# Optimization experiments

Measured on AMD Instinct MI355X. Metric: run time of the kernel, lower is better.

Reference implementation:

```python
import jax, jax.numpy as jnp
import numpy as np

N_NODES = 100000
N_EDGES = 1600000
D_IN = 128
UNITS = 128


def setup_inputs() -> dict:
    key = jax.random.key(0)
    k1, k2, k3, k4, k5 = jax.random.split(key, 5)
    x = jax.random.normal(k1, (N_NODES, D_IN), dtype=jnp.float32)
    # glorot-uniform-like dense weight
    limit = float(np.sqrt(6.0 / (D_IN + UNITS)))
    w = jax.random.uniform(k2, (D_IN, UNITS), minval=-limit, maxval=limit, dtype=jnp.float32)
    # COO sparse adjacency: A[row, col] = val
    edge_row = jax.random.randint(k3, (N_EDGES,), 0, N_NODES, dtype=jnp.int32)
    edge_col = jax.random.randint(k4, (N_EDGES,), 0, N_NODES, dtype=jnp.int32)
    edge_val = jax.random.uniform(k5, (N_EDGES,), dtype=jnp.float32)
    return {"x": x, "w": w, "edge_row": edge_row, "edge_col": edge_col, "edge_val": edge_val}


def reference(x, w, edge_row, edge_col, edge_val):
    # dropout rate = 0.0 -> identity (module default)
    xw = x @ w                                   # [N, units] dense projection
    # sparse adjacency propagation: out[i] = sum_e val[e] * xw[col[e]] for row[e]==i
    msgs = xw[edge_col] * edge_val[:, None]      # [E, units] irregular gather
    out = jax.ops.segment_sum(msgs, edge_row, num_segments=x.shape[0])
    return jax.nn.relu(out)                      # activation
```

## Files before the change

kernel.cpp:

```cpp
#include <hip/hip_runtime.h>

#define N_NODES 100000
#define N_EDGES 1600000
#define D 128
#define NB 512
#define BCAP 3584
#define BSTRIDE 16
#define CHUNK 4000
#define NSCAT 400
#define NGEMM 782
#define HCAP 1792

typedef __attribute__((ext_vector_type(8))) short  short8;
typedef __attribute__((ext_vector_type(4))) float  floatx4;

__device__ __forceinline__ ushort f2bf(float f) {
    unsigned u = __float_as_uint(f);
    u += 0x7FFF + ((u >> 16) & 1);
    return (ushort)(u >> 16);
}
__device__ __forceinline__ float bf2f(ushort s) {
    return __uint_as_float((unsigned)s << 16);
}
__device__ __forceinline__ int bucket_of(int r)  { return (int)(((unsigned)r << 9) / 100000u); }
__device__ __forceinline__ int row_start(int b)  { return (b * 100000 + 511) >> 9; }

__global__ __launch_bounds__(256) void gemm_xw(const float* __restrict__ x,
                                               const float* __restrict__ w,
                                               ushort* __restrict__ xwb) {
    __shared__ ushort wt[128 * 128];
    __shared__ ushort ct[4][16 * 128];
    const int t    = threadIdx.x;
    const int wv   = t >> 6;
    const int lane = t & 63;
    const int m    = lane & 15;
    const int q    = lane >> 4;

    {
        const float4* w4 = (const float4*)w;
        for (int i = t; i < 4096; i += 256) {
            const float4 v = w4[i];
            const int k = i >> 5;
            const int n = (i & 31) << 2;
            const int c = k >> 3, kc = k & 7;
#pragma unroll
            for (int d = 0; d < 4; ++d) {
                const float val = (d == 0) ? v.x : (d == 1) ? v.y : (d == 2) ? v.z : v.w;
                const int nn = n + d;
                wt[(nn << 7) | (((c ^ (nn & 15)) & 15) << 3) | kc] = f2bf(val);
            }
        }
    }
    __syncthreads();

#pragma unroll
    for (int tile = 0; tile < 2; ++tile) {
        const int rbase = blockIdx.x * 128 + tile * 64 + wv * 16;
        if (rbase >= N_NODES) break;

        const float* xrow = x + (size_t)min(rbase + m, N_NODES - 1) * D;

        floatx4 acc[8];
#pragma unroll
        for (int tt = 0; tt < 8; ++tt) acc[tt] = (floatx4){0.f, 0.f, 0.f, 0.f};

#pragma unroll
        for (int kk = 0; kk < D; kk += 32) {
            const float4 a0 = *(const float4*)(xrow + kk + q * 8);
            const float4 a1 = *(const float4*)(xrow + kk + q * 8 + 4);
            short8 a;
            a[0] = (short)f2bf(a0.x); a[1] = (short)f2bf(a0.y);
            a[2] = (short)f2bf(a0.z); a[3] = (short)f2bf(a0.w);
            a[4] = (short)f2bf(a1.x); a[5] = (short)f2bf(a1.y);
            a[6] = (short)f2bf(a1.z); a[7] = (short)f2bf(a1.w);

#pragma unroll
            for (int tt = 0; tt < 8; ++tt) {
                const int n  = tt * 16 + m;
                const int cc = (((kk >> 3) + q) ^ m) & 15;
                const short8 b = *(const short8*)&wt[(n << 7) | (cc << 3)];
                acc[tt] = __builtin_amdgcn_mfma_f32_16x16x32_bf16(a, b, acc[tt], 0, 0, 0);
            }
        }

#pragma unroll
        for (int tt = 0; tt < 8; ++tt) {
#pragma unroll
            for (int r = 0; r < 4; ++r) {
                ct[wv][((q << 2) | r) * 128 + tt * 16 + m] = f2bf(acc[tt][r]);
            }
        }
        const int rl  = lane >> 2;
        const int ch  = lane & 3;
        const int row = rbase + rl;
        if (row < N_NODES) {
            const ushort* srcp = &ct[wv][rl * 128 + ch * 32];
            ushort*       dstp = &xwb[(size_t)row * D + ch * 32];
#pragma unroll
            for (int u = 0; u < 4; ++u) {
                ((int4*)dstp)[u] = ((const int4*)srcp)[u];
            }
        }
    }
}

__global__ __launch_bounds__(256) void bucket_scatter(const int* __restrict__ erow,
                                                      const int* __restrict__ ecol,
                                                      const float* __restrict__ eval,
                                                      int* __restrict__ bcnt,
                                                      int2* __restrict__ bkt) {
    __shared__ int2  stage[CHUNK];
    __shared__ int   sA[NB], sB[NB], lcur[NB], gbase[NB];
    __shared__ short sbuck[CHUNK];
    const int t  = threadIdx.x;
    const int e0 = blockIdx.x * CHUNK;

    sA[t] = 0; sA[t + 256] = 0;
    __syncthreads();

    for (int i = t; i < CHUNK; i += 256) {
        atomicAdd(&sA[bucket_of(erow[e0 + i])], 1);
    }
    __syncthreads();

    int cur = 0;
    int* bufs[2] = {sA, sB};
#pragma unroll
    for (int o = 1; o < 512; o <<= 1) {
        const int* src = bufs[cur];
        int*       dst = bufs[cur ^ 1];
        const int i0 = t, i1 = t + 256;
        dst[i0] = src[i0] + ((i0 >= o) ? src[i0 - o] : 0);
        dst[i1] = src[i1] + ((i1 >= o) ? src[i1 - o] : 0);
        cur ^= 1;
        __syncthreads();
    }
    {
        const int* incl = bufs[cur];
        int*       excl = bufs[cur ^ 1];
        excl[t]       = (t == 0) ? 0 : incl[t - 1];
        excl[t + 256] = incl[t + 255];
    }
    __syncthreads();
    int* L = bufs[cur ^ 1];

    for (int b = t; b < NB; b += 256) {
        lcur[b] = L[b];
        const int cnt = ((b == NB - 1) ? CHUNK : L[b + 1]) - L[b];
        gbase[b] = (cnt > 0) ? atomicAdd(&bcnt[b * BSTRIDE], cnt) : 0;
    }
    __syncthreads();

    for (int i = t; i < CHUNK; i += 256) {
        const int   r = erow[e0 + i];
        const int   c = ecol[e0 + i];
        const float v = eval[e0 + i];
        const int   b = bucket_of(r);
        const int  rl = r - row_start(b);
        const int pos = atomicAdd(&lcur[b], 1);
        stage[pos] = make_int2((rl << 17) | c, __float_as_int(v));
        sbuck[pos] = (short)b;
    }
    __syncthreads();

    for (int i = t; i < CHUNK; i += 256) {
        const int b   = sbuck[i];
        const int dst = gbase[b] + (i - L[b]);
        if (dst < BCAP) bkt[(size_t)b * BCAP + dst] = stage[i];
    }
}

__global__ __launch_bounds__(256, 4) void csr_gather(const int* __restrict__ bcnt,
                                                     const int2* __restrict__ bkt,
                                                     const ushort* __restrict__ xwb,
                                                     float* __restrict__ out) {
    __shared__ int2 lcsr[HCAP];
    __shared__ int  sA[256], sB[256], lcur[256];
    const int bg = blockIdx.x;
    const int b  = bg >> 1;
    const int h  = bg & 1;
    const int t  = threadIdx.x;
    const int n  = min(bcnt[b * BSTRIDE], BCAP);
    const int r0    = row_start(b);
    const int nrows = row_start(b + 1) - r0;
    const int mid   = (nrows + 1) >> 1;
    const int lo    = h ? mid : 0;
    const int hi    = h ? nrows : mid;
    const int nloc  = hi - lo;

    const int2* src = bkt + (size_t)b * BCAP;
    sA[t] = 0;
    __syncthreads();

    for (int i = t; i < n; i += 256) {
        const int rl = (int)(((unsigned)src[i].x) >> 17);
        if (rl >= lo && rl < hi) atomicAdd(&sA[rl - lo], 1);
    }
    __syncthreads();

    int cur = 0;
    int* bufs[2] = {sA, sB};
#pragma unroll
    for (int o = 1; o < 256; o <<= 1) {
        const int* s = bufs[cur];
        int*       d = bufs[cur ^ 1];
        d[t] = s[t] + ((t >= o) ? s[t - o] : 0);
        cur ^= 1;
        __syncthreads();
    }
    lcur[t] = (t == 0) ? 0 : bufs[cur][t - 1];
    __syncthreads();

    for (int i = t; i < n; i += 256) {
        const int2 e = src[i];
        const int rl = (int)(((unsigned)e.x) >> 17);
        if (rl >= lo && rl < hi) {
            const int pos = atomicAdd(&lcur[rl - lo], 1);
            if (pos < HCAP) lcsr[pos] = make_int2(e.x & 0x1FFFF, e.y);
        }
    }
    __syncthreads();

    const int qid = t >> 4;
    const int lc  = (t & 15) << 3;

    for (int ln = qid; ln < nloc; ln += 16) {
        int start = (ln == 0) ? 0 : lcur[ln - 1];
        int end   = lcur[ln];
        start = min(start, HCAP);
        end   = min(end, HCAP);

        float acc[8] = {0, 0, 0, 0, 0, 0, 0, 0};

        for (int j = start; j < end; j += 4) {
            const int jb = j + 1, jc = j + 2, jd = j + 3;
            const int2 e0 = lcsr[j];
            const int2 e1 = lcsr[min(jb, end - 1)];
            const int2 e2 = lcsr[min(jc, end - 1)];
            const int2 e3 = lcsr[min(jd, end - 1)];
            const short8 m0 = *(const short8*)&xwb[(size_t)e0.x * D + lc];
            const short8 m1 = *(const short8*)&xwb[(size_t)e1.x * D + lc];
            const short8 m2 = *(const short8*)&xwb[(size_t)e2.x * D + lc];
            const short8 m3 = *(const short8*)&xwb[(size_t)e3.x * D + lc];
            const float v0 = __int_as_float(e0.y);
            const float v1 = (jb < end) ? __int_as_float(e1.y) : 0.f;
            const float v2 = (jc < end) ? __int_as_float(e2.y) : 0.f;
            const float v3 = (jd < end) ? __int_as_float(e3.y) : 0.f;
#pragma unroll
            for (int i = 0; i < 8; ++i) {
                acc[i] += v0 * bf2f((ushort)m0[i]);
                acc[i] += v1 * bf2f((ushort)m1[i]);
                acc[i] += v2 * bf2f((ushort)m2[i]);
                acc[i] += v3 * bf2f((ushort)m3[i]);
            }
        }

        float* o = out + (size_t)(r0 + lo + ln) * D + lc;
        *(float4*)(o + 0) = make_float4(fmaxf(acc[0], 0.f), fmaxf(acc[1], 0.f),
                                        fmaxf(acc[2], 0.f), fmaxf(acc[3], 0.f));
        *(float4*)(o + 4) = make_float4(fmaxf(acc[4], 0.f), fmaxf(acc[5], 0.f),
                                        fmaxf(acc[6], 0.f), fmaxf(acc[7], 0.f));
    }
}

extern "C" void kernel_launch(void* const* d_in, const int* in_sizes, int n_in,
                              void* d_out, int out_size, void* d_ws, size_t ws_size,
                              hipStream_t stream) {
    const float* x    = (const float*)d_in[0];
    const float* w    = (const float*)d_in[1];
    const int*   erow = (const int*)d_in[2];
    const int*   ecol = (const int*)d_in[3];
    const float* eval = (const float*)d_in[4];
    float*       out  = (float*)d_out;

    char*   ws_base = (char*)d_ws;
    ushort* xwb  = (ushort*)ws_base;
    int*    bcnt = (int*)(ws_base + 25600000);
    int2*   bkt  = (int2*)(ws_base + 25632768);

    (void)hipMemsetAsync(bcnt, 0, 32768, stream);

    gemm_xw<<<NGEMM, 256, 0, stream>>>(x, w, xwb);
    bucket_scatter<<<NSCAT, 256, 0, stream>>>(erow, ecol, eval, bcnt, bkt);
    csr_gather<<<NB * 2, 256, 0, stream>>>(bcnt, bkt, xwb, out);
}
```

Baseline: 232.0 us.

## Reorder to aggregate-then-project: gather bf16 x, then MFMA GEMM per row tile

After: 225.9 us. 1.03x faster.

```diff
diff --git a/kernel.cpp b/kernel.cpp
--- a/kernel.cpp
+++ b/kernel.cpp
@@ -6,9 +6,9 @@
 #define NB 512
 #define BCAP 3584
 #define BSTRIDE 16
-#define CHUNK 4000
-#define NSCAT 400
-#define NGEMM 782
+#define CHUNK 3200
+#define NSCAT 500
+#define NCAST 521
 #define HCAP 1792
 
 typedef __attribute__((ext_vector_type(8))) short  short8;
@@ -25,94 +25,30 @@
 __device__ __forceinline__ int bucket_of(int r)  { return (int)(((unsigned)r << 9) / 100000u); }
 __device__ __forceinline__ int row_start(int b)  { return (b * 100000 + 511) >> 9; }
 
-__global__ __launch_bounds__(256) void gemm_xw(const float* __restrict__ x,
-                                               const float* __restrict__ w,
-                                               ushort* __restrict__ xwb) {
-    __shared__ ushort wt[128 * 128];
-    __shared__ ushort ct[4][16 * 128];
-    const int t    = threadIdx.x;
-    const int wv   = t >> 6;
-    const int lane = t & 63;
-    const int m    = lane & 15;
-    const int q    = lane >> 4;
-
-    {
-        const float4* w4 = (const float4*)w;
-        for (int i = t; i < 4096; i += 256) {
-            const float4 v = w4[i];
-            const int k = i >> 5;
-            const int n = (i & 31) << 2;
-            const int c = k >> 3, kc = k & 7;
-#pragma unroll
-            for (int d = 0; d < 4; ++d) {
-                const float val = (d == 0) ? v.x : (d == 1) ? v.y : (d == 2) ? v.z : v.w;
-                const int nn = n + d;
-                wt[(nn << 7) | (((c ^ (nn & 15)) & 15) << 3) | kc] = f2bf(val);
-            }
-        }
-    }
-    __syncthreads();
-
-#pragma unroll
-    for (int tile = 0; tile < 2; ++tile) {
-        const int rbase = blockIdx.x * 128 + tile * 64 + wv * 16;
-        if (rbase >= N_NODES) break;
-
-        const float* xrow = x + (size_t)min(rbase + m, N_NODES - 1) * D;
-
-        floatx4 acc[8];
-#pragma unroll
-        for (int tt = 0; tt < 8; ++tt) acc[tt] = (floatx4){0.f, 0.f, 0.f, 0.f};
-
-#pragma unroll
-        for (int kk = 0; kk < D; kk += 32) {
-            const float4 a0 = *(const float4*)(xrow + kk + q * 8);
-            const float4 a1 = *(const float4*)(xrow + kk + q * 8 + 4);
-            short8 a;
-            a[0] = (short)f2bf(a0.x); a[1] = (short)f2bf(a0.y);
-            a[2] = (short)f2bf(a0.z); a[3] = (short)f2bf(a0.w);
-            a[4] = (short)f2bf(a1.x); a[5] = (short)f2bf(a1.y);
-            a[6] = (short)f2bf(a1.z); a[7] = (short)f2bf(a1.w);
-
-#pragma unroll
-            for (int tt = 0; tt < 8; ++tt) {
-                const int n  = tt * 16 + m;
-                const int cc = (((kk >> 3) + q) ^ m) & 15;
-                const short8 b = *(const short8*)&wt[(n << 7) | (cc << 3)];
-                acc[tt] = __builtin_amdgcn_mfma_f32_16x16x32_bf16(a, b, acc[tt], 0, 0, 0);
-            }
-        }
-
-#pragma unroll
-        for (int tt = 0; tt < 8; ++tt) {
-#pragma unroll
-            for (int r = 0; r < 4; ++r) {
-                ct[wv][((q << 2) | r) * 128 + tt * 16 + m] = f2bf(acc[tt][r]);
-            }
-        }
-        const int rl  = lane >> 2;
-        const int ch  = lane & 3;
-        const int row = rbase + rl;
-        if (row < N_NODES) {
-            const ushort* srcp = &ct[wv][rl * 128 + ch * 32];
-            ushort*       dstp = &xwb[(size_t)row * D + ch * 32];
-#pragma unroll
-            for (int u = 0; u < 4; ++u) {
-                ((int4*)dstp)[u] = ((const int4*)srcp)[u];
-            }
-        }
-    }
-}
-
-__global__ __launch_bounds__(256) void bucket_scatter(const int* __restrict__ erow,
-                                                      const int* __restrict__ ecol,
-                                                      const float* __restrict__ eval,
-                                                      int* __restrict__ bcnt,
-                                                      int2* __restrict__ bkt) {
+__global__ __launch_bounds__(256, 4) void cast_and_scatter(const float* __restrict__ x,
+                                                           ushort* __restrict__ xb,
+                                                           const int* __restrict__ erow,
+                                                           const int* __restrict__ ecol,
+                                                           const float* __restrict__ eval,
+                                                           int* __restrict__ bcnt,
+                                                           int2* __restrict__ bkt) {
     __shared__ int2  stage[CHUNK];
     __shared__ int   sA[NB], sB[NB], lcur[NB], gbase[NB];
     __shared__ short sbuck[CHUNK];
-    const int t  = threadIdx.x;
+    const int t = threadIdx.x;
+
+    if (blockIdx.x >= NSCAT) {
+        const int gid = (blockIdx.x - NSCAT) * 256 + t;
+        const float4* x4 = (const float4*)x;
+        for (int i = gid; i < (N_NODES * D / 4); i += NCAST * 256) {
+            const float4 v = x4[i];
+            ushort4 o;
+            o.x = f2bf(v.x); o.y = f2bf(v.y); o.z = f2bf(v.z); o.w = f2bf(v.w);
+            ((ushort4*)xb)[i] = o;
+        }
+        return;
+    }
+
     const int e0 = blockIdx.x * CHUNK;
 
     sA[t] = 0; sA[t + 256] = 0;
@@ -170,12 +106,15 @@
     }
 }
 
-__global__ __launch_bounds__(256, 4) void csr_gather(const int* __restrict__ bcnt,
-                                                     const int2* __restrict__ bkt,
-                                                     const ushort* __restrict__ xwb,
-                                                     float* __restrict__ out) {
-    __shared__ int2 lcsr[HCAP];
-    __shared__ int  sA[256], sB[256], lcur[256];
+__global__ __launch_bounds__(256) void gather_gemm(const int* __restrict__ bcnt,
+                                                   const int2* __restrict__ bkt,
+                                                   const ushort* __restrict__ xb,
+                                                   const float* __restrict__ w,
+                                                   float* __restrict__ out) {
+    __shared__ int2   lcsr[HCAP];
+    __shared__ int    sA[256], sB[256], lcur[256];
+    __shared__ ushort wt[128 * 128];
+    __shared__ ushort gbuf[4][16 * 128];
     const int bg = blockIdx.x;
     const int b  = bg >> 1;
     const int h  = bg & 1;
@@ -188,6 +127,24 @@
     const int hi    = h ? nrows : mid;
     const int nloc  = hi - lo;
 
+    {
+        const float4* w4 = (const float4*)w;
+        const int kb    = t & 7;
+        const int ncol4 = t >> 3;
+        const int nc    = ncol4 << 2;
+        for (int it = 0; it < 16; ++it) {
+            const int k = kb + it * 8;
+            const float4 v = w4[k * 32 + ncol4];
+            const int c = k >> 3, kc = k & 7;
+#pragma unroll
+            for (int d = 0; d < 4; ++d) {
+                const float val = (d == 0) ? v.x : (d == 1) ? v.y : (d == 2) ? v.z : v.w;
+                const int nn = nc + d;
+                wt[(nn << 7) | (((c ^ (nn & 15)) & 15) << 3) | kc] = f2bf(val);
+            }
+        }
+    }
+
     const int2* src = bkt + (size_t)b * BCAP;
     sA[t] = 0;
     __syncthreads();
@@ -221,45 +178,91 @@
     }
     __syncthreads();
 
-    const int qid = t >> 4;
-    const int lc  = (t & 15) << 3;
-
-    for (int ln = qid; ln < nloc; ln += 16) {
-        int start = (ln == 0) ? 0 : lcur[ln - 1];
-        int end   = lcur[ln];
-        start = min(start, HCAP);
-        end   = min(end, HCAP);
-
-        float acc[8] = {0, 0, 0, 0, 0, 0, 0, 0};
-
-        for (int j = start; j < end; j += 4) {
-            const int jb = j + 1, jc = j + 2, jd = j + 3;
-            const int2 e0 = lcsr[j];
-            const int2 e1 = lcsr[min(jb, end - 1)];
-            const int2 e2 = lcsr[min(jc, end - 1)];
-            const int2 e3 = lcsr[min(jd, end - 1)];
-            const short8 m0 = *(const short8*)&xwb[(size_t)e0.x * D + lc];
-            const short8 m1 = *(const short8*)&xwb[(size_t)e1.x * D + lc];
-            const short8 m2 = *(const short8*)&xwb[(size_t)e2.x * D + lc];
-            const short8 m3 = *(const short8*)&xwb[(size_t)e3.x * D + lc];
-            const float v0 = __int_as_float(e0.y);
-            const float v1 = (jb < end) ? __int_as_float(e1.y) : 0.f;
-            const float v2 = (jc < end) ? __int_as_float(e2.y) : 0.f;
-            const float v3 = (jd < end) ? __int_as_float(e3.y) : 0.f;
-#pragma unroll
-            for (int i = 0; i < 8; ++i) {
-                acc[i] += v0 * bf2f((ushort)m0[i]);
-                acc[i] += v1 * bf2f((ushort)m1[i]);
-                acc[i] += v2 * bf2f((ushort)m2[i]);
-                acc[i] += v3 * bf2f((ushort)m3[i]);
-            }
-        }
-
-        float* o = out + (size_t)(r0 + lo + ln) * D + lc;
-        *(float4*)(o + 0) = make_float4(fmaxf(acc[0], 0.f), fmaxf(acc[1], 0.f),
-                                        fmaxf(acc[2], 0.f), fmaxf(acc[3], 0.f));
-        *(float4*)(o + 4) = make_float4(fmaxf(acc[4], 0.f), fmaxf(acc[5], 0.f),
-                                        fmaxf(acc[6], 0.f), fmaxf(acc[7], 0.f));
+    const int wv  = t >> 6;
+    const int ln64 = t & 63;
+    const int qq  = ln64 >> 4;
+    const int m16 = ln64 & 15;
+    const int lc  = m16 << 3;
+    ushort* gb = gbuf[wv];
+    const int base_row = wv * 4;
+    const int IT = (nloc > base_row) ? ((nloc - base_row + 15) >> 4) : 0;
+    const int MBN = (IT + 3) >> 2;
+
+    for (int mb = 0; mb < MBN; ++mb) {
+#pragma unroll
+        for (int j = 0; j < 4; ++j) {
+            const int it = mb * 4 + j;
+            const int ln = base_row + qq + 16 * it;
+
+            float acc[8] = {0, 0, 0, 0, 0, 0, 0, 0};
+            if (ln < nloc) {
+                int start = (ln == 0) ? 0 : lcur[ln - 1];
+                int end   = lcur[ln];
+                start = min(start, HCAP);
+                end   = min(end, HCAP);
+
+                for (int jj = start; jj < end; jj += 4) {
+                    const int jb = jj + 1, jc = jj + 2, jd = jj + 3;
+                    const int2 e0 = lcsr[jj];
+                    const int2 e1 = lcsr[min(jb, end - 1)];
+                    const int2 e2 = lcsr[min(jc, end - 1)];
+                    const int2 e3 = lcsr[min(jd, end - 1)];
+                    const short8 m0 = *(const short8*)&xb[(size_t)e0.x * D + lc];
+                    const short8 m1 = *(const short8*)&xb[(size_t)e1.x * D + lc];
+                    const short8 m2 = *(const short8*)&xb[(size_t)e2.x * D + lc];
+                    const short8 m3 = *(const short8*)&xb[(size_t)e3.x * D + lc];
+                    const float v0 = __int_as_float(e0.y);
+                    const float v1 = (jb < end) ? __int_as_float(e1.y) : 0.f;
+                    const float v2 = (jc < end) ? __int_as_float(e2.y) : 0.f;
+                    const float v3 = (jd < end) ? __int_as_float(e3.y) : 0.f;
+#pragma unroll
+                    for (int i = 0; i < 8; ++i) {
+                        acc[i] += v0 * bf2f((ushort)m0[i]);
+                        acc[i] += v1 * bf2f((ushort)m1[i]);
+                        acc[i] += v2 * bf2f((ushort)m2[i]);
+                        acc[i] += v3 * bf2f((ushort)m3[i]);
+                    }
+                }
+            }
+            const int s    = (j << 2) | qq;
+            const int phys = m16 ^ (s & 7);
+            short8 og;
+#pragma unroll
+            for (int i = 0; i < 8; ++i) og[i] = (short)f2bf(acc[i]);
+            *(short8*)&gb[s * 128 + (phys << 3)] = og;
+        }
+
+        short8 afr[4];
+#pragma unroll
+        for (int k2 = 0; k2 < 4; ++k2) {
+            const int ph = (((k2 << 2) | qq) ^ (m16 & 7));
+            afr[k2] = *(const short8*)&gb[m16 * 128 + (ph << 3)];
+        }
+        floatx4 c8[8];
+#pragma unroll
+        for (int tt = 0; tt < 8; ++tt) c8[tt] = (floatx4){0.f, 0.f, 0.f, 0.f};
+#pragma unroll
+        for (int k2 = 0; k2 < 4; ++k2) {
+#pragma unroll
+            for (int tt = 0; tt < 8; ++tt) {
+                const int bn = tt * 16 + m16;
+                const int cc = (((k2 << 2) + qq) ^ m16) & 15;
+                const short8 bb = *(const short8*)&wt[(bn << 7) | (cc << 3)];
+                c8[tt] = __builtin_amdgcn_mfma_f32_16x16x32_bf16(afr[k2], bb, c8[tt], 0, 0, 0);
+            }
+        }
+#pragma unroll
+        for (int r = 0; r < 4; ++r) {
+            const int s2  = (qq << 2) | r;
+            const int ln2 = base_row + (s2 & 3) + 16 * (mb * 4 + (s2 >> 2));
+            if (ln2 < nloc) {
+                float* orow = out + (size_t)(r0 + lo + ln2) * D + m16;
+#pragma unroll
+                for (int tt = 0; tt < 8; ++tt) {
+                    orow[tt * 16] = fmaxf(c8[tt][r], 0.f);
+                }
+            }
+        }
     }
 }
 
@@ -274,13 +277,12 @@
     float*       out  = (float*)d_out;
 
     char*   ws_base = (char*)d_ws;
-    ushort* xwb  = (ushort*)ws_base;
+    ushort* xb   = (ushort*)ws_base;
     int*    bcnt = (int*)(ws_base + 25600000);
     int2*   bkt  = (int2*)(ws_base + 25632768);
 
     (void)hipMemsetAsync(bcnt, 0, 32768, stream);
 
-    gemm_xw<<<NGEMM, 256, 0, stream>>>(x, w, xwb);
-    bucket_scatter<<<NSCAT, 256, 0, stream>>>(erow, ecol, eval, bcnt, bkt);
-    csr_gather<<<NB * 2, 256, 0, stream>>>(bcnt, bkt, xwb, out);
-}
+    cast_and_scatter<<<NSCAT + NCAST, 256, 0, stream>>>(x, xb, erow, ecol, eval, bcnt, bkt);
+    gather_gemm<<<NB * 2, 256, 0, stream>>>(bcnt, bkt, xb, w, out);
+}
```
